# Optimization experiments

Measured on AMD Instinct MI355X. Metric: run time of the kernel, lower is better.

The kernel has to match this reference:

```python
import jax, jax.numpy as jnp
import numpy as np

NUM_HEADS = 8
EMBED_DIM = 128
HEAD_DIM = EMBED_DIM // NUM_HEADS  # 16
NB_FEATURES = EMBED_DIM            # 128
EPS = 1e-4


def _make_projection(nb_rows, nb_cols, rng):
    # gaussian_orthogonal_random_matrix with scaling=0
    blocks = []
    for _ in range(nb_rows // nb_cols):
        q, _ = np.linalg.qr(rng.standard_normal((nb_cols, nb_cols)))
        blocks.append(q.T)
    rem = nb_rows - (nb_rows // nb_cols) * nb_cols
    if rem > 0:
        q, _ = np.linalg.qr(rng.standard_normal((nb_cols, nb_cols)))
        blocks.append(q.T[:rem])
    final = np.concatenate(blocks, axis=0)
    mult = np.linalg.norm(rng.standard_normal((nb_rows, nb_cols)), axis=1)
    return (mult[:, None] * final).astype(np.float32)


def setup_inputs() -> dict:
    key = jax.random.key(0)
    ks = jax.random.split(key, 7)
    R, C, E = 8, 2048, EMBED_DIM
    s = 1.0 / np.sqrt(E)
    x = jax.random.normal(ks[0], (R, C, E), dtype=jnp.float32)
    Wq = jax.random.uniform(ks[1], (E, E), jnp.float32, -s, s)
    bq = jax.random.uniform(ks[2], (E,), jnp.float32, -s, s)
    Wk = jax.random.uniform(ks[3], (E, E), jnp.float32, -s, s)
    bk = jax.random.uniform(ks[4], (E,), jnp.float32, -s, s)
    Wv = jax.random.uniform(ks[5], (E, E), jnp.float32, -s, s)
    bv = jax.random.uniform(ks[6], (E,), jnp.float32, -s, s)
    proj = jnp.asarray(_make_projection(NB_FEATURES, HEAD_DIM, np.random.default_rng(0)))
    return {"x": x, "Wq": Wq, "bq": bq, "Wk": Wk, "bk": bk, "Wv": Wv, "bv": bv, "proj": proj}


def _softmax_kernel(data, proj, is_query):
    # data: (R, h, n, d); proj: (F, d)
    d = data.shape[-1]
    normalizer = d ** (-0.25)
    ratio = proj.shape[0] ** (-0.5)
    data_dash = jnp.einsum('rhnd,jd->rhnj', normalizer * data, proj)  # (R,h,n,F)
    diag = jnp.sum(data * data, axis=-1, keepdims=True) * 0.5 * normalizer ** 2
    if is_query:
        m = jnp.max(data_dash, axis=-1, keepdims=True)
    else:
        m = jnp.max(data_dash, axis=(-1, -2), keepdims=True)
    return ratio * (jnp.exp(data_dash - diag - m) + EPS)


def reference(x, Wq, bq, Wk, bk, Wv, bv, proj):
    R, C, E = x.shape
    h, hd = NUM_HEADS, HEAD_DIM

    def proj_heads(W, b):
        y = jnp.einsum('rce,fe->rcf', x, W) + b
        return y.reshape(R, C, h, hd).transpose(0, 2, 1, 3)  # (R,h,C,hd)

    q = _softmax_kernel(proj_heads(Wq, bq), proj, is_query=True)   # (R,h,C,F)
    k = _softmax_kernel(proj_heads(Wk, bk), proj, is_query=False)  # (R,h,C,F)
    v = proj_heads(Wv, bv)                                          # (R,h,C,hd)

    # fold batch (R) into the feature dim: (h, C, R*F) / (h, C, R*hd)
    qf = q.transpose(1, 2, 0, 3).reshape(h, C, R * NB_FEATURES)
    kf = k.transpose(1, 2, 0, 3).reshape(h, C, R * NB_FEATURES)
    vf = v.transpose(1, 2, 0, 3).reshape(h, C, R * hd)

    k_sum = kf.sum(axis=-2)                                   # (h, D)
    D_inv = 1.0 / jnp.einsum('hnd,hd->hn', qf, k_sum)         # (h, C)
    context = jnp.einsum('hnd,hne->hde', kf, vf)              # (h, D, Ev)
    out = jnp.einsum('hde,hnd,hn->hne', context, qf, D_inv)   # (h, C, R*hd)

    out = out.reshape(h, C, R, hd).transpose(2, 1, 0, 3).reshape(R, C, E)
    attn = jnp.einsum('hqf,hkf->hqk', qf, kf)                 # (h, C, C)
    return out, attn
```

## Files before the change

### kernel.cpp

```cpp
#include <hip/hip_runtime.h>
#include <hip/hip_bf16.h>
#include <stdint.h>

typedef __bf16 bf16x8 __attribute__((ext_vector_type(8)));
typedef float  f32x4  __attribute__((ext_vector_type(4)));

#define RATIO 0.08838834764831845f
#define EPSV  1e-4f

#define GLOBAL_AS __attribute__((address_space(1)))
#define LDS_AS    __attribute__((address_space(3)))

static __device__ __forceinline__ void gload16(const void* g, void* l) {
  __builtin_amdgcn_global_load_lds((GLOBAL_AS const void*)g, (LDS_AS void*)l, 16, 0, 0);
}

static constexpr size_t OFF_XB    = 0;
static constexpr size_t OFF_WCAT  = OFF_XB    + 4194304;
static constexpr size_t OFF_MQ    = OFF_WCAT  + 98304;
static constexpr size_t OFF_MK    = OFF_MQ    + 262144;
static constexpr size_t OFF_BCAT  = OFF_MK    + 262144;
static constexpr size_t OFF_BQF   = OFF_BCAT  + 2048;
static constexpr size_t OFF_BKF   = OFF_BQF   + 4096;
static constexpr size_t OFF_Y     = OFF_BKF   + 4096;
static constexpr size_t OFF_QF    = OFF_Y     + 25165824;
static constexpr size_t OFF_KF    = OFF_QF    + 33554432;
static constexpr size_t OFF_KFT   = OFF_KF    + 33554432;
static constexpr size_t OFF_VFT   = OFF_KFT   + 33554432;
static constexpr size_t OFF_KPART = OFF_VFT   + 4194304;
static constexpr size_t OFF_KMAX  = OFF_KPART + 4096;
static constexpr size_t OFF_KSUM  = OFF_KMAX  + 256;
static constexpr size_t OFF_DINV  = OFF_KSUM  + 32768;
static constexpr size_t OFF_CTXP  = OFF_DINV  + 65536;
static constexpr size_t OFF_CTXT  = OFF_CTXP  + 16777216;
static constexpr size_t WS_NEED   = OFF_CTXT  + 2097152;

static __device__ __forceinline__ void gemm_core(
    const __hip_bfloat16* __restrict__ A, const __hip_bfloat16* __restrict__ B,
    int lda, int ldb, int K, int tm, int tn,
    __bf16* As, __bf16* Bs, f32x4 acc[4][4]) {
  const int t    = threadIdx.x;
  const int w    = t >> 6;
  const int lane = t & 63;
  const int m_off = (w >> 1) << 6;
  const int n_off = (w & 1) << 6;
  const int r0 = t >> 2;
  const int kk = (t & 3) << 3;
  char* Asb = (char*)As + (w << 10);
  char* Bsb = (char*)Bs + (w << 10);
  const int frow = lane & 15;
  const int koff = (lane >> 4) << 3;
  for (int k0 = 0; k0 < K; k0 += 32) {
    const __hip_bfloat16* Ag = A + (size_t)(tm + r0) * lda + (k0 + kk);
    const __hip_bfloat16* Bg = B + (size_t)(tn + r0) * ldb + (k0 + kk);
    gload16(Ag, Asb);
    gload16(Ag + (size_t)64 * lda, Asb + 4096);
    gload16(Bg, Bsb);
    gload16(Bg + (size_t)64 * ldb, Bsb + 4096);
    __syncthreads();
    bf16x8 af[4], bfr[4];
#pragma unroll
    for (int mi = 0; mi < 4; ++mi)
      af[mi] = *(const bf16x8*)(As + ((m_off + mi * 16 + frow) << 5) + koff);
#pragma unroll
    for (int ni = 0; ni < 4; ++ni)
      bfr[ni] = *(const bf16x8*)(Bs + ((n_off + ni * 16 + frow) << 5) + koff);
#pragma unroll
    for (int mi = 0; mi < 4; ++mi)
#pragma unroll
      for (int ni = 0; ni < 4; ++ni)
        acc[mi][ni] = __builtin_amdgcn_mfma_f32_16x16x32_bf16(af[mi], bfr[ni], acc[mi][ni], 0, 0, 0);
    __syncthreads();
  }
}

#define ZERO_ACC(acc) do {                                   \
  _Pragma("unroll") for (int a_ = 0; a_ < 4; ++a_)           \
  _Pragma("unroll") for (int b_ = 0; b_ < 4; ++b_)           \
    acc[a_][b_] = (f32x4){0.f, 0.f, 0.f, 0.f};               \
} while (0)

__global__ void k_prep(const float* __restrict__ x,
                       const float* __restrict__ Wq, const float* __restrict__ bq,
                       const float* __restrict__ Wk, const float* __restrict__ bk,
                       const float* __restrict__ Wv, const float* __restrict__ bv,
                       const float* __restrict__ proj,
                       __hip_bfloat16* __restrict__ xb,
                       __hip_bfloat16* __restrict__ Wcat, float* __restrict__ bcat,
                       __hip_bfloat16* __restrict__ Mq, __hip_bfloat16* __restrict__ Mk,
                       float* __restrict__ bqf, float* __restrict__ bkf) {
  const int b = blockIdx.x, t = threadIdx.x;
  {
    int i = (b * 256 + t) * 4;
    f32x4 v = *(const f32x4*)(x + i);
#pragma unroll
    for (int j = 0; j < 4; ++j) xb[i + j] = __float2bfloat16(v[j]);
  }
  if (b < 1024) {
    int i = b * 256 + t;
    {
      int which = i >> 17;
      int rem = i & 131071;
      int hj = rem >> 7, e = rem & 127;
      int hh = hj >> 7, j = hj & 127;
      const float* W = which ? Wk : Wq;
      float s = 0.f;
#pragma unroll
      for (int u = 0; u < 16; ++u) s += proj[j * 16 + u] * W[(hh * 16 + u) * 128 + e];
      if (which) Mk[rem] = __float2bfloat16(0.5f * s);
      else       Mq[rem] = __float2bfloat16(0.5f * s);
    }
    if (i < 2048) {
      int which = i >> 10;
      int hj = i & 1023, hh = hj >> 7, j = hj & 127;
      const float* bb = which ? bk : bq;
      float s = 0.f;
#pragma unroll
      for (int u = 0; u < 16; ++u) s += proj[j * 16 + u] * bb[hh * 16 + u];
      if (which) bkf[hj] = 0.5f * s;
      else       bqf[hj] = 0.5f * s;
    }
  }
  if (b < 192) {
    int i = b * 256 + t;
    int mat = i >> 14, rem = i & 16383;
    const float* W = (mat == 0) ? Wq : ((mat == 1) ? Wk : Wv);
    Wcat[i] = __float2bfloat16(W[rem]);
    if (i < 384) {
      int m2 = i >> 7;
      const float* bb = (m2 == 0) ? bq : ((m2 == 1) ? bk : bv);
      bcat[i] = bb[i & 127];
    }
  }
}

__global__ __launch_bounds__(256) void k_proj(
    const __hip_bfloat16* __restrict__ xb, const __hip_bfloat16* __restrict__ Wcat,
    const float* __restrict__ bcat, float* __restrict__ Y) {
  __shared__ __align__(16) __bf16 As[4096], Bs[4096];
  const int tm = blockIdx.x << 7, tn = blockIdx.y << 7;
  f32x4 acc[4][4];
  ZERO_ACC(acc);
  gemm_core(xb, Wcat, 128, 128, 128, tm, tn, As, Bs, acc);
  const int t = threadIdx.x, w = t >> 6, lane = t & 63;
  const int m_off = (w >> 1) << 6, n_off = (w & 1) << 6;
#pragma unroll
  for (int ni = 0; ni < 4; ++ni) {
    const int col = tn + n_off + ni * 16 + (lane & 15);
    const float bias = bcat[col];
#pragma unroll
    for (int mi = 0; mi < 4; ++mi)
#pragma unroll
      for (int i = 0; i < 4; ++i) {
        const int row = tm + m_off + mi * 16 + ((lane >> 4) << 2) + i;
        Y[(size_t)row * 384 + col] = acc[mi][ni][i] + bias;
      }
  }
}

__global__ void k_vft2(const float* __restrict__ Y, __hip_bfloat16* __restrict__ vfT) {
  const int cb = blockIdx.x, r = blockIdx.y, h = blockIdx.z;
  const int c0 = cb << 7;
  __shared__ float tile[16][132];
  const int t = threadIdx.x;
  const int a = t & 15, cc0 = t >> 4;
#pragma unroll
  for (int i = 0; i < 8; ++i) {
    const int cc = cc0 + (i << 4);
    tile[a][cc] = Y[(size_t)(r * 2048 + c0 + cc) * 384 + 256 + (h << 4) + a];
  }
  __syncthreads();
  const int row = t >> 4, cg = t & 15;
  bf16x8 v;
#pragma unroll
  for (int j = 0; j < 8; ++j) v[j] = (__bf16)tile[row][(cg << 3) + j];
  *(bf16x8*)(vfT + ((size_t)((h << 7) + (r << 4) + row) << 11) + c0 + (cg << 3)) = v;
}

__global__ __launch_bounds__(256) void k_dashq(
    const __hip_bfloat16* __restrict__ xb, const __hip_bfloat16* __restrict__ Mq,
    const float* __restrict__ bqf, const float* __restrict__ Y,
    __hip_bfloat16* __restrict__ qf) {
  __shared__ __align__(16) __bf16 As[4096], Bs[4096];
  __shared__ float diag_s[128];
  __shared__ float rmax_s[2][128];
  const int h = blockIdx.y;
  const int tm = blockIdx.x << 7;
  f32x4 acc[4][4];
  ZERO_ACC(acc);
  gemm_core(xb, Mq + h * 16384, 128, 128, 128, tm, 0, As, Bs, acc);
  const int t = threadIdx.x, w = t >> 6, lane = t & 63;
  const int m_off = (w >> 1) << 6, n_off = (w & 1) << 6;
  if (t < 128) {
    const float* yp = Y + (size_t)(tm + t) * 384 + h * 16;
    float s = 0.f;
#pragma unroll
    for (int u = 0; u < 16; ++u) s += yp[u] * yp[u];
    diag_s[t] = 0.125f * s;
  }
  float bia[4];
#pragma unroll
  for (int ni = 0; ni < 4; ++ni) bia[ni] = bqf[h * 128 + n_off + ni * 16 + (lane & 15)];
  float rmx[4][4];
#pragma unroll
  for (int mi = 0; mi < 4; ++mi)
#pragma unroll
    for (int i = 0; i < 4; ++i) {
      float m0 = acc[mi][0][i] + bia[0];
      m0 = fmaxf(m0, acc[mi][1][i] + bia[1]);
      m0 = fmaxf(m0, acc[mi][2][i] + bia[2]);
      m0 = fmaxf(m0, acc[mi][3][i] + bia[3]);
      rmx[mi][i] = m0;
    }
#pragma unroll
  for (int off = 1; off < 16; off <<= 1)
#pragma unroll
    for (int mi = 0; mi < 4; ++mi)
#pragma unroll
      for (int i = 0; i < 4; ++i)
        rmx[mi][i] = fmaxf(rmx[mi][i], __shfl_xor(rmx[mi][i], off));
  if ((lane & 15) == 0) {
#pragma unroll
    for (int mi = 0; mi < 4; ++mi)
#pragma unroll
      for (int i = 0; i < 4; ++i)
        rmax_s[w & 1][m_off + mi * 16 + ((lane >> 4) << 2) + i] = rmx[mi][i];
  }
  __syncthreads();
#pragma unroll
  for (int mi = 0; mi < 4; ++mi) {
#pragma unroll
    for (int i = 0; i < 4; ++i) {
      const int rl = m_off + mi * 16 + ((lane >> 4) << 2) + i;
      const int rg = tm + rl;
      const int c = rg & 2047, r = rg >> 11;
      const float md = diag_s[rl] + fmaxf(rmax_s[0][rl], rmax_s[1][rl]);
#pragma unroll
      for (int ni = 0; ni < 4; ++ni) {
        const int j = n_off + ni * 16 + (lane & 15);
        const float f = RATIO * (__expf(acc[mi][ni][i] + bia[ni] - md) + EPSV);
        qf[((size_t)((h << 11) + c) << 10) + (r << 7) + j] = __float2bfloat16(f);
      }
    }
  }
}

__global__ __launch_bounds__(256) void k_dashk_max(
    const __hip_bfloat16* __restrict__ xb, const __hip_bfloat16* __restrict__ Mk,
    const float* __restrict__ bkf, float* __restrict__ kpart) {
  __shared__ __align__(16) __bf16 As[4096], Bs[4096];
  __shared__ float wmax[4];
  const int h = blockIdx.y;
  const int tm = blockIdx.x << 7;
  f32x4 acc[4][4];
  ZERO_ACC(acc);
  gemm_core(xb, Mk + h * 16384, 128, 128, 128, tm, 0, As, Bs, acc);
  const int t = threadIdx.x, w = t >> 6, lane = t & 63;
  const int n_off = (w & 1) << 6;
  float mx = -1e30f;
#pragma unroll
  for (int ni = 0; ni < 4; ++ni) {
    const float bia = bkf[h * 128 + n_off + ni * 16 + (lane & 15)];
#pragma unroll
    for (int mi = 0; mi < 4; ++mi)
#pragma unroll
      for (int i = 0; i < 4; ++i) mx = fmaxf(mx, acc[mi][ni][i] + bia);
  }
#pragma unroll
  for (int off = 1; off < 64; off <<= 1) mx = fmaxf(mx, __shfl_xor(mx, off));
  if (lane == 0) wmax[w] = mx;
  __syncthreads();
  if (t == 0) kpart[h * 128 + blockIdx.x] = fmaxf(fmaxf(wmax[0], wmax[1]), fmaxf(wmax[2], wmax[3]));
}

__global__ void k_kmaxred(const float* __restrict__ kpart, float* __restrict__ kmax) {
  const int t = threadIdx.x;
  const int r = t >> 3, h = t & 7;
  float m = -1e30f;
  for (int i = 0; i < 16; ++i) m = fmaxf(m, kpart[h * 128 + r * 16 + i]);
  kmax[r * 8 + h] = m;
}

__global__ __launch_bounds__(256) void k_dashk_feat(
    const __hip_bfloat16* __restrict__ xb, const __hip_bfloat16* __restrict__ Mk,
    const float* __restrict__ bkf, const float* __restrict__ Y,
    const float* __restrict__ kmax,
    __hip_bfloat16* __restrict__ kf, __hip_bfloat16* __restrict__ kfT) {
  __shared__ __align__(16) __bf16 As[4096], Bs[4096];
  __shared__ float diag_s[128];
  __shared__ __align__(16) __bf16 kT[128 * 136];
  const int h = blockIdx.y;
  const int tm = blockIdx.x << 7;
  f32x4 acc[4][4];
  ZERO_ACC(acc);
  gemm_core(xb, Mk + h * 16384, 128, 128, 128, tm, 0, As, Bs, acc);
  const int t = threadIdx.x, w = t >> 6, lane = t & 63;
  const int m_off = (w >> 1) << 6, n_off = (w & 1) << 6;
  if (t < 128) {
    const float* yp = Y + (size_t)(tm + t) * 384 + 128 + h * 16;
    float s = 0.f;
#pragma unroll
    for (int u = 0; u < 16; ++u) s += yp[u] * yp[u];
    diag_s[t] = 0.125f * s;
  }
  const int r = tm >> 11;
  const int c0 = tm & 2047;
  const float m = kmax[r * 8 + h];
  float bia[4];
#pragma unroll
  for (int ni = 0; ni < 4; ++ni) bia[ni] = bkf[h * 128 + n_off + ni * 16 + (lane & 15)];
  __syncthreads();
#pragma unroll
  for (int mi = 0; mi < 4; ++mi) {
#pragma unroll
    for (int i = 0; i < 4; ++i) {
      const int rl = m_off + mi * 16 + ((lane >> 4) << 2) + i;
      const int c = c0 + rl;
      const float dm = diag_s[rl] + m;
#pragma unroll
      for (int ni = 0; ni < 4; ++ni) {
        const int j = n_off + ni * 16 + (lane & 15);
        const float f = RATIO * (__expf(acc[mi][ni][i] + bia[ni] - dm) + EPSV);
        kf[((size_t)((h << 11) + c) << 10) + (r << 7) + j] = __float2bfloat16(f);
        kT[j * 136 + rl] = (__bf16)f;
      }
    }
  }
  __syncthreads();
  const int j2 = t >> 1, half = t & 1;
  __bf16* dst = (__bf16*)kfT + (((size_t)(h << 10) + (r << 7) + j2) << 11) + c0 + (half << 6);
  const __bf16* srcr = kT + j2 * 136 + (half << 6);
#pragma unroll
  for (int q8 = 0; q8 < 8; ++q8)
    *(bf16x8*)(dst + (q8 << 3)) = *(const bf16x8*)(srcr + (q8 << 3));
}

__global__ __launch_bounds__(256) void k_ksum2(const __hip_bfloat16* __restrict__ kfT,
                                               float* __restrict__ ksum) {
  const int t = threadIdx.x, w = t >> 6, lane = t & 63;
  const int row = blockIdx.x * 4 + w;
  const __bf16* p = (const __bf16*)kfT + ((size_t)row << 11);
  float s = 0.f;
#pragma unroll
  for (int q = 0; q < 4; ++q) {
    bf16x8 v = *(const bf16x8*)(p + ((lane + (q << 6)) << 3));
#pragma unroll
    for (int j = 0; j < 8; ++j) s += (float)v[j];
  }
#pragma unroll
  for (int off = 1; off < 64; off <<= 1) s += __shfl_xor(s, off);
  if (lane == 0) ksum[row] = s;
}

__global__ __launch_bounds__(256) void k_dinv(
    const __hip_bfloat16* __restrict__ qf, const float* __restrict__ ksum,
    float* __restrict__ dinv) {
  const int t = threadIdx.x, w = t >> 6, lane = t & 63;
  const int h = blockIdx.y;
  const int c = blockIdx.x * 4 + w;
  const __bf16* qp = (const __bf16*)qf + ((size_t)((h << 11) + c) << 10);
  const float* ks = ksum + h * 1024;
  const int d0 = lane << 4;
  bf16x8 v0 = *(const bf16x8*)(qp + d0);
  bf16x8 v1 = *(const bf16x8*)(qp + d0 + 8);
  float s = 0.f;
#pragma unroll
  for (int j = 0; j < 8; ++j) s += (float)v0[j] * ks[d0 + j] + (float)v1[j] * ks[d0 + 8 + j];
#pragma unroll
  for (int off = 1; off < 64; off <<= 1) s += __shfl_xor(s, off);
  if (lane == 0) dinv[(h << 11) + c] = 1.0f / s;
}

#define SBAR() __builtin_amdgcn_s_barrier()
#define FEN()  do { asm volatile("" ::: "memory"); __builtin_amdgcn_sched_barrier(0); } while (0)
#define PRIO1() __builtin_amdgcn_s_setprio(1)
#define PRIO0() __builtin_amdgcn_s_setprio(0)
#define VMW4() do { asm volatile("s_waitcnt vmcnt(4)" ::: "memory"); } while (0)
#define VMW0() do { asm volatile("s_waitcnt vmcnt(0)" ::: "memory"); } while (0)

#define MFMA16(nlo) do {                                                      \
  _Pragma("unroll") for (int mi_ = 0; mi_ < 8; ++mi_)                         \
  _Pragma("unroll") for (int nj_ = 0; nj_ < 2; ++nj_)                         \
    acc[mi_][(nlo) + nj_] = __builtin_amdgcn_mfma_f32_16x16x32_bf16(          \
        aR[mi_], bR[nj_], acc[mi_][(nlo) + nj_], 0, 0, 0);                    \
} while (0)

__global__ __launch_bounds__(512, 2) void k_attn8(
    const __hip_bfloat16* __restrict__ qf, const __hip_bfloat16* __restrict__ kf,
    float* __restrict__ attn) {
  extern __shared__ __align__(128) char lds[];
  const int lid = blockIdx.x;
  const int swz = ((lid & 7) << 6) + (lid >> 3);
  const int h  = swz >> 6;
  const int tm = ((swz >> 3) & 7) << 8;
  const int tn = (swz & 7) << 8;
  const __hip_bfloat16* Ag = qf + ((size_t)h << 21);
  const __hip_bfloat16* Bg = kf + ((size_t)h << 21);

  const int t = threadIdx.x, wid = t >> 6, lane = t & 63;
  const int f = lane & 15;
  const int wr = wid >> 2, wc = wid & 3;
  const int swzg = (((lane >> 4) ^ ((f >> 1) & 3)) << 4);
  const int aoff = ((wr << 7) + f) * 64 + swzg;
  const int boff = 65536 + ((wc << 6) + f) * 64 + swzg;
  const int srow = t >> 2;
  const int scol = (((t & 3) ^ ((t >> 3) & 3)) << 3);
  const int sdst = wid << 10;

  f32x4 acc[8][4] = {};
  bf16x8 aR[8], bR[2];

  auto stageA = [&](int buf, int kh, int k0) {
    char* d = lds + buf * 32768 + kh * 16384 + sdst;
    const __hip_bfloat16* g = Ag + (size_t)(tm + srow) * 1024 + k0 + (kh << 5) + scol;
    gload16(g, d);
    gload16(g + 128 * 1024, d + 8192);
  };
  auto stageB = [&](int buf, int kh, int k0) {
    char* d = lds + 65536 + buf * 32768 + kh * 16384 + sdst;
    const __hip_bfloat16* g = Bg + (size_t)(tn + srow) * 1024 + k0 + (kh << 5) + scol;
    gload16(g, d);
    gload16(g + 128 * 1024, d + 8192);
  };

  stageA(0, 0, 0); stageB(0, 0, 0); stageA(0, 1, 0); stageB(0, 1, 0);
  VMW4();
  SBAR(); FEN();

  for (int kt = 0; kt < 15; ++kt) {
    const int buf = kt & 1, nbuf = buf ^ 1;
    const int bo = buf * 32768;
    const int nk0 = (kt + 1) << 6;
#pragma unroll
    for (int mi = 0; mi < 8; ++mi) aR[mi] = *(const bf16x8*)(lds + bo + aoff + mi * 1024);
    bR[0] = *(const bf16x8*)(lds + bo + boff);
    bR[1] = *(const bf16x8*)(lds + bo + boff + 1024);
    stageA(nbuf, 0, nk0);
    PRIO1(); MFMA16(0); PRIO0();
    SBAR(); FEN();
    bR[0] = *(const bf16x8*)(lds + bo + boff + 2048);
    bR[1] = *(const bf16x8*)(lds + bo + boff + 3072);
    stageB(nbuf, 0, nk0);
    PRIO1(); MFMA16(2); PRIO0();
    VMW4();
    SBAR(); FEN();
#pragma unroll
    for (int mi = 0; mi < 8; ++mi) aR[mi] = *(const bf16x8*)(lds + bo + 16384 + aoff + mi * 1024);
    bR[0] = *(const bf16x8*)(lds + bo + 16384 + boff);
    bR[1] = *(const bf16x8*)(lds + bo + 16384 + boff + 1024);
    stageA(nbuf, 1, nk0);
    PRIO1(); MFMA16(0); PRIO0();
    SBAR(); FEN();
    bR[0] = *(const bf16x8*)(lds + bo + 16384 + boff + 2048);
    bR[1] = *(const bf16x8*)(lds + bo + 16384 + boff + 3072);
    stageB(nbuf, 1, nk0);
    PRIO1(); MFMA16(2); PRIO0();
    VMW4();
    SBAR(); FEN();
  }
  {
    const int bo = 32768;
#pragma unroll
    for (int mi = 0; mi < 8; ++mi) aR[mi] = *(const bf16x8*)(lds + bo + aoff + mi * 1024);
    bR[0] = *(const bf16x8*)(lds + bo + boff);
    bR[1] = *(const bf16x8*)(lds + bo + boff + 1024);
    PRIO1(); MFMA16(0); PRIO0();
    bR[0] = *(const bf16x8*)(lds + bo + boff + 2048);
    bR[1] = *(const bf16x8*)(lds + bo + boff + 3072);
    PRIO1(); MFMA16(2); PRIO0();
    VMW0();
    SBAR(); FEN();
#pragma unroll
    for (int mi = 0; mi < 8; ++mi) aR[mi] = *(const bf16x8*)(lds + bo + 16384 + aoff + mi * 1024);
    bR[0] = *(const bf16x8*)(lds + bo + 16384 + boff);
    bR[1] = *(const bf16x8*)(lds + bo + 16384 + boff + 1024);
    PRIO1(); MFMA16(0); PRIO0();
    bR[0] = *(const bf16x8*)(lds + bo + 16384 + boff + 2048);
    bR[1] = *(const bf16x8*)(lds + bo + 16384 + boff + 3072);
    PRIO1(); MFMA16(2); PRIO0();
  }

  float* Cc = attn + ((size_t)h << 22);
  const int rbase = tm + (wr << 7) + ((lane >> 4) << 2);
  const int cbase = tn + (wc << 6) + f;
#pragma unroll
  for (int mi = 0; mi < 8; ++mi)
#pragma unroll
    for (int i = 0; i < 4; ++i) {
      float* rp = Cc + ((size_t)(rbase + mi * 16 + i) << 11) + cbase;
#pragma unroll
      for (int ni = 0; ni < 4; ++ni) rp[ni * 16] = acc[mi][ni][i];
    }
}

__global__ __launch_bounds__(256) void k_ctx(
    const __hip_bfloat16* __restrict__ vfT, const __hip_bfloat16* __restrict__ kfT,
    float* __restrict__ ctxp) {
  __shared__ __align__(16) __bf16 As[4096], Bs[4096];
  const int z = blockIdx.z, h = z >> 2, kc = z & 3;
  const int tn = blockIdx.y << 7;
  f32x4 acc[4][4];
  ZERO_ACC(acc);
  gemm_core(vfT + ((size_t)h << 18) + (kc << 9), kfT + ((size_t)h << 21) + (kc << 9),
            2048, 2048, 512, 0, tn, As, Bs, acc);
  float* Cp = ctxp + ((size_t)(kc * 8 + h) << 17);
  const int t = threadIdx.x, w = t >> 6, lane = t & 63;
  const int m_off = (w >> 1) << 6, n_off = (w & 1) << 6;
#pragma unroll
  for (int mi = 0; mi < 4; ++mi)
#pragma unroll
    for (int i = 0; i < 4; ++i) {
      const int row = m_off + mi * 16 + ((lane >> 4) << 2) + i;
#pragma unroll
      for (int ni = 0; ni < 4; ++ni) {
        const int col = tn + n_off + ni * 16 + (lane & 15);
        Cp[((size_t)row << 10) + col] = acc[mi][ni][i];
      }
    }
}

__global__ void k_ctxred(const float* __restrict__ ctxp, __hip_bfloat16* __restrict__ ctxT) {
  const int i = blockIdx.x * 256 + threadIdx.x;
  const float s = ctxp[i] + ctxp[i + 1048576] + ctxp[i + 2097152] + ctxp[i + 3145728];
  ctxT[i] = __float2bfloat16(s);
}

__global__ __launch_bounds__(256) void k_out(
    const __hip_bfloat16* __restrict__ qf, const __hip_bfloat16* __restrict__ ctxT,
    const float* __restrict__ dinv, float* __restrict__ outp) {
  __shared__ __align__(16) __bf16 As[4096], Bs[4096];
  const int h = blockIdx.z;
  const int tm = blockIdx.x << 7;
  f32x4 acc[4][4];
  ZERO_ACC(acc);
  gemm_core(qf + ((size_t)h << 21), ctxT + ((size_t)h << 17), 1024, 1024, 1024, tm, 0, As, Bs, acc);
  const int t = threadIdx.x, w = t >> 6, lane = t & 63;
  const int m_off = (w >> 1) << 6, n_off = (w & 1) << 6;
#pragma unroll
  for (int mi = 0; mi < 4; ++mi)
#pragma unroll
    for (int i = 0; i < 4; ++i) {
      const int row = tm + m_off + mi * 16 + ((lane >> 4) << 2) + i;
      const float dv = dinv[(h << 11) + row];
#pragma unroll
      for (int ni = 0; ni < 4; ++ni) {
        const int col = n_off + ni * 16 + (lane & 15);
        const int rb = col >> 4, tt = col & 15;
        outp[(((size_t)(rb << 11) + row) << 7) + (h << 4) + tt] = acc[mi][ni][i] * dv;
      }
    }
}

extern "C" void kernel_launch(void* const* d_in, const int* in_sizes, int n_in,
                              void* d_out, int out_size, void* d_ws, size_t ws_size,
                              hipStream_t stream) {
  const float* x    = (const float*)d_in[0];
  const float* Wq   = (const float*)d_in[1];
  const float* bq   = (const float*)d_in[2];
  const float* Wk   = (const float*)d_in[3];
  const float* bk   = (const float*)d_in[4];
  const float* Wv   = (const float*)d_in[5];
  const float* bv   = (const float*)d_in[6];
  const float* proj = (const float*)d_in[7];
  if (ws_size < WS_NEED) return;

  char* ws = (char*)d_ws;
  __hip_bfloat16* xb   = (__hip_bfloat16*)(ws + OFF_XB);
  __hip_bfloat16* Wcat = (__hip_bfloat16*)(ws + OFF_WCAT);
  __hip_bfloat16* Mq   = (__hip_bfloat16*)(ws + OFF_MQ);
  __hip_bfloat16* Mk   = (__hip_bfloat16*)(ws + OFF_MK);
  float* bcat = (float*)(ws + OFF_BCAT);
  float* bqf  = (float*)(ws + OFF_BQF);
  float* bkf  = (float*)(ws + OFF_BKF);
  float* Y    = (float*)(ws + OFF_Y);
  __hip_bfloat16* qf  = (__hip_bfloat16*)(ws + OFF_QF);
  __hip_bfloat16* kf  = (__hip_bfloat16*)(ws + OFF_KF);
  __hip_bfloat16* kfT = (__hip_bfloat16*)(ws + OFF_KFT);
  __hip_bfloat16* vfT = (__hip_bfloat16*)(ws + OFF_VFT);
  float* kpart = (float*)(ws + OFF_KPART);
  float* kmax  = (float*)(ws + OFF_KMAX);
  float* ksum  = (float*)(ws + OFF_KSUM);
  float* dinv  = (float*)(ws + OFF_DINV);
  float* ctxp  = (float*)(ws + OFF_CTXP);
  __hip_bfloat16* ctxT = (__hip_bfloat16*)(ws + OFF_CTXT);

  float* outp = (float*)d_out;
  float* attn = (float*)d_out + 2097152;

  static int attr_done = 0;
  if (!attr_done) {
    (void)hipFuncSetAttribute((const void*)k_attn8,
                              hipFuncAttributeMaxDynamicSharedMemorySize, 131072);
    attr_done = 1;
  }

  k_prep<<<dim3(2048), dim3(256), 0, stream>>>(x, Wq, bq, Wk, bk, Wv, bv, proj,
                                               xb, Wcat, bcat, Mq, Mk, bqf, bkf);
  k_proj<<<dim3(128, 3), dim3(256), 0, stream>>>(xb, Wcat, bcat, Y);
  k_vft2<<<dim3(16, 8, 8), dim3(256), 0, stream>>>(Y, vfT);
  k_dashq<<<dim3(128, 8), dim3(256), 0, stream>>>(xb, Mq, bqf, Y, qf);
  k_dashk_max<<<dim3(128, 8), dim3(256), 0, stream>>>(xb, Mk, bkf, kpart);
  k_kmaxred<<<dim3(1), dim3(64), 0, stream>>>(kpart, kmax);
  k_dashk_feat<<<dim3(128, 8), dim3(256), 0, stream>>>(xb, Mk, bkf, Y, kmax, kf, kfT);
  k_ksum2<<<dim3(2048), dim3(256), 0, stream>>>(kfT, ksum);
  k_dinv<<<dim3(512, 8), dim3(256), 0, stream>>>(qf, ksum, dinv);
  k_attn8<<<dim3(512), dim3(512), 131072, stream>>>(qf, kf, attn);
  k_ctx<<<dim3(1, 8, 32), dim3(256), 0, stream>>>(vfT, kfT, ctxp);
  k_ctxred<<<dim3(4096), dim3(256), 0, stream>>>(ctxp, ctxT);
  k_out<<<dim3(16, 1, 8), dim3(256), 0, stream>>>(qf, ctxT, dinv, outp);
}
```

Measured before the change: 201.5 us.

## Stage dashq output through LDS for coalesced stores; merge attn MFMA half-phases

In k_dashq the bf16 qf values are first written into a padded LDS tile, then copied out as 16-byte vector stores per row, replacing scattered 2-byte global writes. The diag computation is also moved ahead of the GEMM. In k_attn8 each k-half now loads all four B fragments at once and issues one 32-MFMA block with a single barrier, instead of two 16-MFMA phases separated by a barrier. The aim is fewer barriers and less interleaving overhead, at the cost of more live registers and less overlap between stage loads and compute. The extra syncthreads and the LDS reuse in dashq add a small cost.

New measurement: 205.8 us. +2.2%, slower.

```diff
diff --git a/kernel.cpp b/kernel.cpp
--- a/kernel.cpp
+++ b/kernel.cpp
@@ -181,16 +181,17 @@
     const __hip_bfloat16* __restrict__ xb, const __hip_bfloat16* __restrict__ Mq,
     const float* __restrict__ bqf, const float* __restrict__ Y,
     __hip_bfloat16* __restrict__ qf) {
-  __shared__ __align__(16) __bf16 As[4096], Bs[4096];
+  __shared__ __align__(16) char pool[34816];
   __shared__ float diag_s[128];
   __shared__ float rmax_s[2][128];
+  __bf16* As = (__bf16*)pool;
+  __bf16* Bs = (__bf16*)(pool + 8192);
+  __bf16* qC = (__bf16*)pool;
   const int h = blockIdx.y;
   const int tm = blockIdx.x << 7;
   f32x4 acc[4][4];
   ZERO_ACC(acc);
-  gemm_core(xb, Mq + h * 16384, 128, 128, 128, tm, 0, As, Bs, acc);
-  const int t = threadIdx.x, w = t >> 6, lane = t & 63;
-  const int m_off = (w >> 1) << 6, n_off = (w & 1) << 6;
+  const int t = threadIdx.x, w = t >> 6, lane = t & 63;
   if (t < 128) {
     const float* yp = Y + (size_t)(tm + t) * 384 + h * 16;
     float s = 0.f;
@@ -198,6 +199,8 @@
     for (int u = 0; u < 16; ++u) s += yp[u] * yp[u];
     diag_s[t] = 0.125f * s;
   }
+  gemm_core(xb, Mq + h * 16384, 128, 128, 128, tm, 0, As, Bs, acc);
+  const int m_off = (w >> 1) << 6, n_off = (w & 1) << 6;
   float bia[4];
 #pragma unroll
   for (int ni = 0; ni < 4; ++ni) bia[ni] = bqf[h * 128 + n_off + ni * 16 + (lane & 15)];
@@ -232,16 +235,23 @@
 #pragma unroll
     for (int i = 0; i < 4; ++i) {
       const int rl = m_off + mi * 16 + ((lane >> 4) << 2) + i;
-      const int rg = tm + rl;
-      const int c = rg & 2047, r = rg >> 11;
       const float md = diag_s[rl] + fmaxf(rmax_s[0][rl], rmax_s[1][rl]);
 #pragma unroll
       for (int ni = 0; ni < 4; ++ni) {
         const int j = n_off + ni * 16 + (lane & 15);
         const float f = RATIO * (__expf(acc[mi][ni][i] + bia[ni] - md) + EPSV);
-        qf[((size_t)((h << 11) + c) << 10) + (r << 7) + j] = __float2bfloat16(f);
+        qC[rl * 136 + j] = (__bf16)f;
       }
     }
+  }
+  __syncthreads();
+  const int r = tm >> 11, c0 = tm & 2047;
+  const int cl0 = t >> 4, j0 = (t & 15) << 3;
+#pragma unroll
+  for (int p = 0; p < 8; ++p) {
+    const int cl = cl0 + (p << 4);
+    bf16x8 v = *(const bf16x8*)(qC + cl * 136 + j0);
+    *(bf16x8*)((__bf16*)qf + (((size_t)((h << 11) + c0 + cl)) << 10) + (r << 7) + j0) = v;
   }
 }
 
@@ -378,11 +388,11 @@
 #define VMW4() do { asm volatile("s_waitcnt vmcnt(4)" ::: "memory"); } while (0)
 #define VMW0() do { asm volatile("s_waitcnt vmcnt(0)" ::: "memory"); } while (0)
 
-#define MFMA16(nlo) do {                                                      \
+#define MFMA32() do {                                                         \
   _Pragma("unroll") for (int mi_ = 0; mi_ < 8; ++mi_)                         \
-  _Pragma("unroll") for (int nj_ = 0; nj_ < 2; ++nj_)                         \
-    acc[mi_][(nlo) + nj_] = __builtin_amdgcn_mfma_f32_16x16x32_bf16(          \
-        aR[mi_], bR[nj_], acc[mi_][(nlo) + nj_], 0, 0, 0);                    \
+  _Pragma("unroll") for (int nj_ = 0; nj_ < 4; ++nj_)                         \
+    acc[mi_][nj_] = __builtin_amdgcn_mfma_f32_16x16x32_bf16(                  \
+        aR[mi_], bR[nj_], acc[mi_][nj_], 0, 0, 0);                            \
 } while (0)
 
 __global__ __launch_bounds__(512, 2) void k_attn8(
@@ -408,7 +418,7 @@
   const int sdst = wid << 10;
 
   f32x4 acc[8][4] = {};
-  bf16x8 aR[8], bR[2];
+  bf16x8 aR[8], bR[4];
 
   auto stageA = [&](int buf, int kh, int k0) {
     char* d = lds + buf * 32768 + kh * 16384 + sdst;
@@ -433,28 +443,20 @@
     const int nk0 = (kt + 1) << 6;
 #pragma unroll
     for (int mi = 0; mi < 8; ++mi) aR[mi] = *(const bf16x8*)(lds + bo + aoff + mi * 1024);
-    bR[0] = *(const bf16x8*)(lds + bo + boff);
-    bR[1] = *(const bf16x8*)(lds + bo + boff + 1024);
+#pragma unroll
+    for (int nj = 0; nj < 4; ++nj) bR[nj] = *(const bf16x8*)(lds + bo + boff + nj * 1024);
     stageA(nbuf, 0, nk0);
-    PRIO1(); MFMA16(0); PRIO0();
-    SBAR(); FEN();
-    bR[0] = *(const bf16x8*)(lds + bo + boff + 2048);
-    bR[1] = *(const bf16x8*)(lds + bo + boff + 3072);
     stageB(nbuf, 0, nk0);
-    PRIO1(); MFMA16(2); PRIO0();
+    PRIO1(); MFMA32(); PRIO0();
     VMW4();
     SBAR(); FEN();
 #pragma unroll
     for (int mi = 0; mi < 8; ++mi) aR[mi] = *(const bf16x8*)(lds + bo + 16384 + aoff + mi * 1024);
-    bR[0] = *(const bf16x8*)(lds + bo + 16384 + boff);
-    bR[1] = *(const bf16x8*)(lds + bo + 16384 + boff + 1024);
+#pragma unroll
+    for (int nj = 0; nj < 4; ++nj) bR[nj] = *(const bf16x8*)(lds + bo + 16384 + boff + nj * 1024);
     stageA(nbuf, 1, nk0);
-    PRIO1(); MFMA16(0); PRIO0();
-    SBAR(); FEN();
-    bR[0] = *(const bf16x8*)(lds + bo + 16384 + boff + 2048);
-    bR[1] = *(const bf16x8*)(lds + bo + 16384 + boff + 3072);
     stageB(nbuf, 1, nk0);
-    PRIO1(); MFMA16(2); PRIO0();
+    PRIO1(); MFMA32(); PRIO0();
     VMW4();
     SBAR(); FEN();
   }
@@ -462,22 +464,16 @@
     const int bo = 32768;
 #pragma unroll
     for (int mi = 0; mi < 8; ++mi) aR[mi] = *(const bf16x8*)(lds + bo + aoff + mi * 1024);
-    bR[0] = *(const bf16x8*)(lds + bo + boff);
-    bR[1] = *(const bf16x8*)(lds + bo + boff + 1024);
-    PRIO1(); MFMA16(0); PRIO0();
-    bR[0] = *(const bf16x8*)(lds + bo + boff + 2048);
-    bR[1] = *(const bf16x8*)(lds + bo + boff + 3072);
-    PRIO1(); MFMA16(2); PRIO0();
+#pragma unroll
+    for (int nj = 0; nj < 4; ++nj) bR[nj] = *(const bf16x8*)(lds + bo + boff + nj * 1024);
+    PRIO1(); MFMA32(); PRIO0();
     VMW0();
     SBAR(); FEN();
 #pragma unroll
     for (int mi = 0; mi < 8; ++mi) aR[mi] = *(const bf16x8*)(lds + bo + 16384 + aoff + mi * 1024);
-    bR[0] = *(const bf16x8*)(lds + bo + 16384 + boff);
-    bR[1] = *(const bf16x8*)(lds + bo + 16384 + boff + 1024);
-    PRIO1(); MFMA16(0); PRIO0();
-    bR[0] = *(const bf16x8*)(lds + bo + 16384 + boff + 2048);
-    bR[1] = *(const bf16x8*)(lds + bo + 16384 + boff + 3072);
-    PRIO1(); MFMA16(2); PRIO0();
+#pragma unroll
+    for (int nj = 0; nj < 4; ++nj) bR[nj] = *(const bf16x8*)(lds + bo + 16384 + boff + nj * 1024);
+    PRIO1(); MFMA32(); PRIO0();
   }
 
   float* Cc = attn + ((size_t)h << 22);
```

## Fuse V transpose, k-sum and D-inverse reductions into producer GEMM epilogues

Applied to the files above, without the earlier changes.

The V-transpose kernel is folded into the projection GEMM's epilogue, which writes vfT through LDS. Per-block k feature sums are accumulated in the key feature kernel. The query feature kernel, now launched after the key kernel, computes partial normalizer dot products, and the output kernel finishes the D inverse. This removes three small kernels (k_vft2, k_ksum2, k_dinv) and their extra passes over kfT and qf. In exchange the epilogues and LDS use of the producer kernels grow, and the q features must wait on the key pass.

After: 191.1 us. -5.2%, faster.

```diff
diff --git a/kernel.cpp b/kernel.cpp
--- a/kernel.cpp
+++ b/kernel.cpp
@@ -29,9 +29,9 @@
 static constexpr size_t OFF_VFT   = OFF_KFT   + 33554432;
 static constexpr size_t OFF_KPART = OFF_VFT   + 4194304;
 static constexpr size_t OFF_KMAX  = OFF_KPART + 4096;
-static constexpr size_t OFF_KSUM  = OFF_KMAX  + 256;
-static constexpr size_t OFF_DINV  = OFF_KSUM  + 32768;
-static constexpr size_t OFF_CTXP  = OFF_DINV  + 65536;
+static constexpr size_t OFF_KSPART= OFF_KMAX  + 1024;
+static constexpr size_t OFF_DPART = OFF_KSPART+ 524288;
+static constexpr size_t OFF_CTXP  = OFF_DPART + 524288;
 static constexpr size_t OFF_CTXT  = OFF_CTXP  + 16777216;
 static constexpr size_t WS_NEED   = OFF_CTXT  + 2097152;
 
@@ -136,111 +136,53 @@
 
 __global__ __launch_bounds__(256) void k_proj(
     const __hip_bfloat16* __restrict__ xb, const __hip_bfloat16* __restrict__ Wcat,
-    const float* __restrict__ bcat, float* __restrict__ Y) {
-  __shared__ __align__(16) __bf16 As[4096], Bs[4096];
+    const float* __restrict__ bcat, float* __restrict__ Y,
+    __hip_bfloat16* __restrict__ vfT) {
+  __shared__ __align__(16) char pool[34816];
+  __bf16* As = (__bf16*)pool;
+  __bf16* Bs = (__bf16*)(pool + 8192);
   const int tm = blockIdx.x << 7, tn = blockIdx.y << 7;
   f32x4 acc[4][4];
   ZERO_ACC(acc);
   gemm_core(xb, Wcat, 128, 128, 128, tm, tn, As, Bs, acc);
   const int t = threadIdx.x, w = t >> 6, lane = t & 63;
   const int m_off = (w >> 1) << 6, n_off = (w & 1) << 6;
-#pragma unroll
-  for (int ni = 0; ni < 4; ++ni) {
-    const int col = tn + n_off + ni * 16 + (lane & 15);
-    const float bias = bcat[col];
-#pragma unroll
-    for (int mi = 0; mi < 4; ++mi)
-#pragma unroll
-      for (int i = 0; i < 4; ++i) {
-        const int row = tm + m_off + mi * 16 + ((lane >> 4) << 2) + i;
-        Y[(size_t)row * 384 + col] = acc[mi][ni][i] + bias;
-      }
-  }
-}
-
-__global__ void k_vft2(const float* __restrict__ Y, __hip_bfloat16* __restrict__ vfT) {
-  const int cb = blockIdx.x, r = blockIdx.y, h = blockIdx.z;
-  const int c0 = cb << 7;
-  __shared__ float tile[16][132];
-  const int t = threadIdx.x;
-  const int a = t & 15, cc0 = t >> 4;
-#pragma unroll
-  for (int i = 0; i < 8; ++i) {
-    const int cc = cc0 + (i << 4);
-    tile[a][cc] = Y[(size_t)(r * 2048 + c0 + cc) * 384 + 256 + (h << 4) + a];
-  }
-  __syncthreads();
-  const int row = t >> 4, cg = t & 15;
-  bf16x8 v;
-#pragma unroll
-  for (int j = 0; j < 8; ++j) v[j] = (__bf16)tile[row][(cg << 3) + j];
-  *(bf16x8*)(vfT + ((size_t)((h << 7) + (r << 4) + row) << 11) + c0 + (cg << 3)) = v;
-}
-
-__global__ __launch_bounds__(256) void k_dashq(
-    const __hip_bfloat16* __restrict__ xb, const __hip_bfloat16* __restrict__ Mq,
-    const float* __restrict__ bqf, const float* __restrict__ Y,
-    __hip_bfloat16* __restrict__ qf) {
-  __shared__ __align__(16) __bf16 As[4096], Bs[4096];
-  __shared__ float diag_s[128];
-  __shared__ float rmax_s[2][128];
-  const int h = blockIdx.y;
-  const int tm = blockIdx.x << 7;
-  f32x4 acc[4][4];
-  ZERO_ACC(acc);
-  gemm_core(xb, Mq + h * 16384, 128, 128, 128, tm, 0, As, Bs, acc);
-  const int t = threadIdx.x, w = t >> 6, lane = t & 63;
-  const int m_off = (w >> 1) << 6, n_off = (w & 1) << 6;
-  if (t < 128) {
-    const float* yp = Y + (size_t)(tm + t) * 384 + h * 16;
-    float s = 0.f;
-#pragma unroll
-    for (int u = 0; u < 16; ++u) s += yp[u] * yp[u];
-    diag_s[t] = 0.125f * s;
-  }
-  float bia[4];
-#pragma unroll
-  for (int ni = 0; ni < 4; ++ni) bia[ni] = bqf[h * 128 + n_off + ni * 16 + (lane & 15)];
-  float rmx[4][4];
-#pragma unroll
-  for (int mi = 0; mi < 4; ++mi)
-#pragma unroll
-    for (int i = 0; i < 4; ++i) {
-      float m0 = acc[mi][0][i] + bia[0];
-      m0 = fmaxf(m0, acc[mi][1][i] + bia[1]);
-      m0 = fmaxf(m0, acc[mi][2][i] + bia[2]);
-      m0 = fmaxf(m0, acc[mi][3][i] + bia[3]);
-      rmx[mi][i] = m0;
-    }
-#pragma unroll
-  for (int off = 1; off < 16; off <<= 1)
-#pragma unroll
-    for (int mi = 0; mi < 4; ++mi)
-#pragma unroll
-      for (int i = 0; i < 4; ++i)
-        rmx[mi][i] = fmaxf(rmx[mi][i], __shfl_xor(rmx[mi][i], off));
-  if ((lane & 15) == 0) {
-#pragma unroll
-    for (int mi = 0; mi < 4; ++mi)
-#pragma unroll
-      for (int i = 0; i < 4; ++i)
-        rmax_s[w & 1][m_off + mi * 16 + ((lane >> 4) << 2) + i] = rmx[mi][i];
-  }
-  __syncthreads();
-#pragma unroll
-  for (int mi = 0; mi < 4; ++mi) {
-#pragma unroll
-    for (int i = 0; i < 4; ++i) {
-      const int rl = m_off + mi * 16 + ((lane >> 4) << 2) + i;
-      const int rg = tm + rl;
-      const int c = rg & 2047, r = rg >> 11;
-      const float md = diag_s[rl] + fmaxf(rmax_s[0][rl], rmax_s[1][rl]);
-#pragma unroll
-      for (int ni = 0; ni < 4; ++ni) {
-        const int j = n_off + ni * 16 + (lane & 15);
-        const float f = RATIO * (__expf(acc[mi][ni][i] + bia[ni] - md) + EPSV);
-        qf[((size_t)((h << 11) + c) << 10) + (r << 7) + j] = __float2bfloat16(f);
-      }
+  const int frow = lane & 15;
+  if (tn == 256) {
+    __bf16* vT = (__bf16*)pool;
+#pragma unroll
+    for (int ni = 0; ni < 4; ++ni) {
+      const int j = n_off + ni * 16 + frow;
+      const float bias = bcat[256 + j];
+#pragma unroll
+      for (int mi = 0; mi < 4; ++mi)
+#pragma unroll
+        for (int i = 0; i < 4; ++i) {
+          const int rl = m_off + mi * 16 + ((lane >> 4) << 2) + i;
+          vT[j * 136 + rl] = (__bf16)(acc[mi][ni][i] + bias);
+        }
+    }
+    __syncthreads();
+    const int r = tm >> 11, c0 = tm & 2047;
+    const int j2 = t >> 1, half = t & 1;
+    const int hh = j2 >> 4, aa = j2 & 15;
+    __bf16* dst = (__bf16*)vfT + (((size_t)(hh * 128 + r * 16 + aa)) << 11) + c0 + (half << 6);
+    const __bf16* srcr = vT + j2 * 136 + (half << 6);
+#pragma unroll
+    for (int q8 = 0; q8 < 8; ++q8)
+      *(bf16x8*)(dst + (q8 << 3)) = *(const bf16x8*)(srcr + (q8 << 3));
+  } else {
+#pragma unroll
+    for (int ni = 0; ni < 4; ++ni) {
+      const int col = tn + n_off + ni * 16 + frow;
+      const float bias = bcat[col];
+#pragma unroll
+      for (int mi = 0; mi < 4; ++mi)
+#pragma unroll
+        for (int i = 0; i < 4; ++i) {
+          const int row = tm + m_off + mi * 16 + ((lane >> 4) << 2) + i;
+          Y[(size_t)row * 384 + col] = acc[mi][ni][i] + bias;
+        }
     }
   }
 }
@@ -285,10 +227,12 @@
     const __hip_bfloat16* __restrict__ xb, const __hip_bfloat16* __restrict__ Mk,
     const float* __restrict__ bkf, const float* __restrict__ Y,
     const float* __restrict__ kmax,
-    __hip_bfloat16* __restrict__ kf, __hip_bfloat16* __restrict__ kfT) {
+    __hip_bfloat16* __restrict__ kf, __hip_bfloat16* __restrict__ kfT,
+    float* __restrict__ kspart) {
   __shared__ __align__(16) __bf16 As[4096], Bs[4096];
   __shared__ float diag_s[128];
   __shared__ __align__(16) __bf16 kT[128 * 136];
+  __shared__ float ksp_s[2][128];
   const int h = blockIdx.y;
   const int tm = blockIdx.x << 7;
   f32x4 acc[4][4];
@@ -296,6 +240,7 @@
   gemm_core(xb, Mk + h * 16384, 128, 128, 128, tm, 0, As, Bs, acc);
   const int t = threadIdx.x, w = t >> 6, lane = t & 63;
   const int m_off = (w >> 1) << 6, n_off = (w & 1) << 6;
+  const int frow = lane & 15;
   if (t < 128) {
     const float* yp = Y + (size_t)(tm + t) * 384 + 128 + h * 16;
     float s = 0.f;
@@ -305,10 +250,12 @@
   }
   const int r = tm >> 11;
   const int c0 = tm & 2047;
+  const int cb = blockIdx.x & 15;
   const float m = kmax[r * 8 + h];
   float bia[4];
 #pragma unroll
-  for (int ni = 0; ni < 4; ++ni) bia[ni] = bkf[h * 128 + n_off + ni * 16 + (lane & 15)];
+  for (int ni = 0; ni < 4; ++ni) bia[ni] = bkf[h * 128 + n_off + ni * 16 + frow];
+  float ksp[4] = {0.f, 0.f, 0.f, 0.f};
   __syncthreads();
 #pragma unroll
   for (int mi = 0; mi < 4; ++mi) {
@@ -319,14 +266,28 @@
       const float dm = diag_s[rl] + m;
 #pragma unroll
       for (int ni = 0; ni < 4; ++ni) {
-        const int j = n_off + ni * 16 + (lane & 15);
+        const int j = n_off + ni * 16 + frow;
         const float f = RATIO * (__expf(acc[mi][ni][i] + bia[ni] - dm) + EPSV);
-        kf[((size_t)((h << 11) + c) << 10) + (r << 7) + j] = __float2bfloat16(f);
+        const __hip_bfloat16 hb = __float2bfloat16(f);
+        kf[((size_t)((h << 11) + c) << 10) + (r << 7) + j] = hb;
         kT[j * 136 + rl] = (__bf16)f;
+        ksp[ni] += __bfloat162float(hb);
       }
     }
   }
+#pragma unroll
+  for (int ni = 0; ni < 4; ++ni) {
+    ksp[ni] += __shfl_xor(ksp[ni], 16);
+    ksp[ni] += __shfl_xor(ksp[ni], 32);
+  }
+  if ((lane >> 4) == 0) {
+#pragma unroll
+    for (int ni = 0; ni < 4; ++ni)
+      ksp_s[w >> 1][n_off + ni * 16 + frow] = ksp[ni];
+  }
   __syncthreads();
+  if (t < 128)
+    kspart[(((cb << 3) + h) << 10) + r * 128 + t] = ksp_s[0][t] + ksp_s[1][t];
   const int j2 = t >> 1, half = t & 1;
   __bf16* dst = (__bf16*)kfT + (((size_t)(h << 10) + (r << 7) + j2) << 11) + c0 + (half << 6);
   const __bf16* srcr = kT + j2 * 136 + (half << 6);
@@ -335,40 +296,103 @@
     *(bf16x8*)(dst + (q8 << 3)) = *(const bf16x8*)(srcr + (q8 << 3));
 }
 
-__global__ __launch_bounds__(256) void k_ksum2(const __hip_bfloat16* __restrict__ kfT,
-                                               float* __restrict__ ksum) {
+__global__ __launch_bounds__(256) void k_dashq(
+    const __hip_bfloat16* __restrict__ xb, const __hip_bfloat16* __restrict__ Mq,
+    const float* __restrict__ bqf, const float* __restrict__ Y,
+    const float* __restrict__ kspart,
+    __hip_bfloat16* __restrict__ qf, float* __restrict__ dpart) {
+  __shared__ __align__(16) __bf16 As[4096], Bs[4096];
+  __shared__ float diag_s[128];
+  __shared__ float rmax_s[2][128];
+  __shared__ float ksum_s[128];
+  __shared__ float dred_s[2][128];
+  const int h = blockIdx.y;
+  const int tm = blockIdx.x << 7;
+  const int r = tm >> 11, c0 = tm & 2047;
+  f32x4 acc[4][4];
+  ZERO_ACC(acc);
   const int t = threadIdx.x, w = t >> 6, lane = t & 63;
-  const int row = blockIdx.x * 4 + w;
-  const __bf16* p = (const __bf16*)kfT + ((size_t)row << 11);
-  float s = 0.f;
-#pragma unroll
-  for (int q = 0; q < 4; ++q) {
-    bf16x8 v = *(const bf16x8*)(p + ((lane + (q << 6)) << 3));
-#pragma unroll
-    for (int j = 0; j < 8; ++j) s += (float)v[j];
-  }
-#pragma unroll
-  for (int off = 1; off < 64; off <<= 1) s += __shfl_xor(s, off);
-  if (lane == 0) ksum[row] = s;
-}
-
-__global__ __launch_bounds__(256) void k_dinv(
-    const __hip_bfloat16* __restrict__ qf, const float* __restrict__ ksum,
-    float* __restrict__ dinv) {
-  const int t = threadIdx.x, w = t >> 6, lane = t & 63;
-  const int h = blockIdx.y;
-  const int c = blockIdx.x * 4 + w;
-  const __bf16* qp = (const __bf16*)qf + ((size_t)((h << 11) + c) << 10);
-  const float* ks = ksum + h * 1024;
-  const int d0 = lane << 4;
-  bf16x8 v0 = *(const bf16x8*)(qp + d0);
-  bf16x8 v1 = *(const bf16x8*)(qp + d0 + 8);
-  float s = 0.f;
-#pragma unroll
-  for (int j = 0; j < 8; ++j) s += (float)v0[j] * ks[d0 + j] + (float)v1[j] * ks[d0 + 8 + j];
-#pragma unroll
-  for (int off = 1; off < 64; off <<= 1) s += __shfl_xor(s, off);
-  if (lane == 0) dinv[(h << 11) + c] = 1.0f / s;
+  if (t < 128) {
+    const float* yp = Y + (size_t)(tm + t) * 384 + h * 16;
+    float s = 0.f;
+#pragma unroll
+    for (int u = 0; u < 16; ++u) s += yp[u] * yp[u];
+    diag_s[t] = 0.125f * s;
+    float ks = 0.f;
+#pragma unroll
+    for (int cb = 0; cb < 16; ++cb) ks += kspart[(((cb << 3) + h) << 10) + r * 128 + t];
+    ksum_s[t] = ks;
+  }
+  gemm_core(xb, Mq + h * 16384, 128, 128, 128, tm, 0, As, Bs, acc);
+  const int m_off = (w >> 1) << 6, n_off = (w & 1) << 6;
+  const int frow = lane & 15;
+  float bia[4];
+#pragma unroll
+  for (int ni = 0; ni < 4; ++ni) bia[ni] = bqf[h * 128 + n_off + ni * 16 + frow];
+  float rmx[4][4];
+#pragma unroll
+  for (int mi = 0; mi < 4; ++mi)
+#pragma unroll
+    for (int i = 0; i < 4; ++i) {
+      float m0 = acc[mi][0][i] + bia[0];
+      m0 = fmaxf(m0, acc[mi][1][i] + bia[1]);
+      m0 = fmaxf(m0, acc[mi][2][i] + bia[2]);
+      m0 = fmaxf(m0, acc[mi][3][i] + bia[3]);
+      rmx[mi][i] = m0;
+    }
+#pragma unroll
+  for (int off = 1; off < 16; off <<= 1)
+#pragma unroll
+    for (int mi = 0; mi < 4; ++mi)
+#pragma unroll
+      for (int i = 0; i < 4; ++i)
+        rmx[mi][i] = fmaxf(rmx[mi][i], __shfl_xor(rmx[mi][i], off));
+  if (frow == 0) {
+#pragma unroll
+    for (int mi = 0; mi < 4; ++mi)
+#pragma unroll
+      for (int i = 0; i < 4; ++i)
+        rmax_s[w & 1][m_off + mi * 16 + ((lane >> 4) << 2) + i] = rmx[mi][i];
+  }
+  __syncthreads();
+  float p[4][4];
+#pragma unroll
+  for (int mi = 0; mi < 4; ++mi)
+#pragma unroll
+    for (int i = 0; i < 4; ++i) p[mi][i] = 0.f;
+#pragma unroll
+  for (int mi = 0; mi < 4; ++mi) {
+#pragma unroll
+    for (int i = 0; i < 4; ++i) {
+      const int rl = m_off + mi * 16 + ((lane >> 4) << 2) + i;
+      const float md = diag_s[rl] + fmaxf(rmax_s[0][rl], rmax_s[1][rl]);
+#pragma unroll
+      for (int ni = 0; ni < 4; ++ni) {
+        const int j = n_off + ni * 16 + frow;
+        const float f = RATIO * (__expf(acc[mi][ni][i] + bia[ni] - md) + EPSV);
+        const __hip_bfloat16 hb = __float2bfloat16(f);
+        qf[((size_t)((h << 11) + c0 + rl) << 10) + (r << 7) + j] = hb;
+        p[mi][i] += __bfloat162float(hb) * ksum_s[j];
+      }
+    }
+  }
+#pragma unroll
+  for (int off = 1; off < 16; off <<= 1)
+#pragma unroll
+    for (int mi = 0; mi < 4; ++mi)
+#pragma unroll
+      for (int i = 0; i < 4; ++i)
+        p[mi][i] += __shfl_xor(p[mi][i], off);
+  if (frow == 0) {
+#pragma unroll
+    for (int mi = 0; mi < 4; ++mi)
+#pragma unroll
+      for (int i = 0; i < 4; ++i)
+        dred_s[w & 1][m_off + mi * 16 + ((lane >> 4) << 2) + i] = p[mi][i];
+  }
+  __syncthreads();
+  if (t < 128)
+    dpart[(((r << 3) + h) << 11) + c0 + t] = dred_s[0][t] + dred_s[1][t];
 }
 
 #define SBAR() __builtin_amdgcn_s_barrier()
@@ -527,21 +551,29 @@
 
 __global__ __launch_bounds__(256) void k_out(
     const __hip_bfloat16* __restrict__ qf, const __hip_bfloat16* __restrict__ ctxT,
-    const float* __restrict__ dinv, float* __restrict__ outp) {
+    const float* __restrict__ dpart, float* __restrict__ outp) {
   __shared__ __align__(16) __bf16 As[4096], Bs[4096];
+  __shared__ float dinv_s[128];
   const int h = blockIdx.z;
   const int tm = blockIdx.x << 7;
+  const int t = threadIdx.x, w = t >> 6, lane = t & 63;
+  if (t < 128) {
+    float s = 0.f;
+#pragma unroll
+    for (int r = 0; r < 8; ++r) s += dpart[(((r << 3) + h) << 11) + tm + t];
+    dinv_s[t] = 1.0f / s;
+  }
   f32x4 acc[4][4];
   ZERO_ACC(acc);
   gemm_core(qf + ((size_t)h << 21), ctxT + ((size_t)h << 17), 1024, 1024, 1024, tm, 0, As, Bs, acc);
-  const int t = threadIdx.x, w = t >> 6, lane = t & 63;
   const int m_off = (w >> 1) << 6, n_off = (w & 1) << 6;
 #pragma unroll
   for (int mi = 0; mi < 4; ++mi)
 #pragma unroll
     for (int i = 0; i < 4; ++i) {
-      const int row = tm + m_off + mi * 16 + ((lane >> 4) << 2) + i;
-      const float dv = dinv[(h << 11) + row];
+      const int rl = m_off + mi * 16 + ((lane >> 4) << 2) + i;
+      const int row = tm + rl;
+      const float dv = dinv_s[rl];
 #pragma unroll
       for (int ni = 0; ni < 4; ++ni) {
         const int col = n_off + ni * 16 + (lane & 15);
@@ -577,11 +609,11 @@
   __hip_bfloat16* kf  = (__hip_bfloat16*)(ws + OFF_KF);
   __hip_bfloat16* kfT = (__hip_bfloat16*)(ws + OFF_KFT);
   __hip_bfloat16* vfT = (__hip_bfloat16*)(ws + OFF_VFT);
-  float* kpart = (float*)(ws + OFF_KPART);
-  float* kmax  = (float*)(ws + OFF_KMAX);
-  float* ksum  = (float*)(ws + OFF_KSUM);
-  float* dinv  = (float*)(ws + OFF_DINV);
-  float* ctxp  = (float*)(ws + OFF_CTXP);
+  float* kpart  = (float*)(ws + OFF_KPART);
+  float* kmax   = (float*)(ws + OFF_KMAX);
+  float* kspart = (float*)(ws + OFF_KSPART);
+  float* dpart  = (float*)(ws + OFF_DPART);
+  float* ctxp   = (float*)(ws + OFF_CTXP);
   __hip_bfloat16* ctxT = (__hip_bfloat16*)(ws + OFF_CTXT);
 
   float* outp = (float*)d_out;
@@ -596,16 +628,13 @@
 
   k_prep<<<dim3(2048), dim3(256), 0, stream>>>(x, Wq, bq, Wk, bk, Wv, bv, proj,
                                                xb, Wcat, bcat, Mq, Mk, bqf, bkf);
-  k_proj<<<dim3(128, 3), dim3(256), 0, stream>>>(xb, Wcat, bcat, Y);
-  k_vft2<<<dim3(16, 8, 8), dim3(256), 0, stream>>>(Y, vfT);
-  k_dashq<<<dim3(128, 8), dim3(256), 0, stream>>>(xb, Mq, bqf, Y, qf);
+  k_proj<<<dim3(128, 3), dim3(256), 0, stream>>>(xb, Wcat, bcat, Y, vfT);
   k_dashk_max<<<dim3(128, 8), dim3(256), 0, stream>>>(xb, Mk, bkf, kpart);
   k_kmaxred<<<dim3(1), dim3(64), 0, stream>>>(kpart, kmax);
-  k_dashk_feat<<<dim3(128, 8), dim3(256), 0, stream>>>(xb, Mk, bkf, Y, kmax, kf, kfT);
-  k_ksum2<<<dim3(2048), dim3(256), 0, stream>>>(kfT, ksum);
-  k_dinv<<<dim3(512, 8), dim3(256), 0, stream>>>(qf, ksum, dinv);
+  k_dashk_feat<<<dim3(128, 8), dim3(256), 0, stream>>>(xb, Mk, bkf, Y, kmax, kf, kfT, kspart);
+  k_dashq<<<dim3(128, 8), dim3(256), 0, stream>>>(xb, Mq, bqf, Y, kspart, qf, dpart);
   k_attn8<<<dim3(512), dim3(512), 131072, stream>>>(qf, kf, attn);
   k_ctx<<<dim3(1, 8, 32), dim3(256), 0, stream>>>(vfT, kfT, ctxp);
   k_ctxred<<<dim3(4096), dim3(256), 0, stream>>>(ctxp, ctxT);
-  k_out<<<dim3(16, 1, 8), dim3(256), 0, stream>>>(qf, ctxT, dinv, outp);
-}
+  k_out<<<dim3(16, 1, 8), dim3(256), 0, stream>>>(qf, ctxT, dpart, outp);
+}
```
